# Performance work log

Measured on AMD Instinct MI355X. Metric: run time of the kernel, lower is better.

The kernel has to match this reference:

```python
import jax, jax.numpy as jnp
import numpy as np


def _gcn_conv(x, W, b, src, dst, norm, n_nodes):
    # PyG GCNConv: h = x @ W, then symmetric-normalized aggregation, then + b
    h = x @ W                                   # [N, F_out]
    msg = h[src] * norm[:, None]                # gather + scale, [E', F_out]
    agg = jax.ops.segment_sum(msg, dst, num_segments=n_nodes)
    return agg + b


def _norm_and_loops(edge_index, n_nodes):
    # add self-loops, compute D^{-1/2} (A+I) D^{-1/2} edge weights
    loop = jnp.arange(n_nodes, dtype=edge_index.dtype)
    src = jnp.concatenate([edge_index[0], loop])
    dst = jnp.concatenate([edge_index[1], loop])
    deg = jax.ops.segment_sum(jnp.ones_like(dst, dtype=jnp.float32), dst,
                              num_segments=n_nodes)
    dinv = jnp.where(deg > 0, jax.lax.rsqrt(deg), 0.0)
    norm = dinv[src] * dinv[dst]
    return src, dst, norm


def setup_inputs() -> dict:
    key = jax.random.key(0)
    ks = jax.random.split(key, 4)
    N, E, n_latent, n_dim = 50000, 800000, 128, 128
    hidden = 2 * n_latent
    x = jax.random.normal(ks[0], (N, n_latent), dtype=jnp.float32)
    edge_index = jax.random.randint(ks[1], (2, E), 0, N, dtype=jnp.int64)
    W1 = jax.random.normal(ks[2], (n_latent, hidden), dtype=jnp.float32) / np.sqrt(n_latent)
    b1 = jnp.zeros((hidden,), dtype=jnp.float32)
    W2 = jax.random.normal(ks[3], (hidden, n_dim), dtype=jnp.float32) / np.sqrt(hidden)
    b2 = jnp.zeros((n_dim,), dtype=jnp.float32)
    return {"x": x, "edge_index": edge_index, "W1": W1, "b1": b1,
            "W2": W2, "b2": b2}


def reference(x, edge_index, W1, b1, W2, b2):
    n_nodes = x.shape[0]
    src, dst, norm = _norm_and_loops(edge_index, n_nodes)
    z1 = jax.nn.relu(_gcn_conv(x, W1, b1, src, dst, norm, n_nodes))
    z2 = _gcn_conv(z1, W2, b2, src, dst, norm, n_nodes)
    return z2
```

## Files before the change

kernel.cpp:

```cpp
#include <hip/hip_runtime.h>


constexpr int F = 128;
constexpr int HID = 256;
constexpr int ECHUNK = 8192;

typedef __attribute__((ext_vector_type(8))) _Float16 f16x8;
typedef __attribute__((ext_vector_type(4))) _Float16 f16x4;
typedef __attribute__((ext_vector_type(2))) _Float16 f16x2;
typedef __attribute__((ext_vector_type(4))) float f32x4;

__global__ __launch_bounds__(256) void k_bzero(unsigned* bcnt) {
  bcnt[threadIdx.x] = 0u;
}

__global__ __launch_bounds__(256) void k_binc(const int* __restrict__ dst,
                                              unsigned* __restrict__ bcnt,
                                              unsigned* __restrict__ bhist, int E) {
  __shared__ unsigned hist[256];
  int tid = threadIdx.x;
  hist[tid] = 0u;
  __syncthreads();
  int i0 = blockIdx.x * ECHUNK;
  int i1 = min(i0 + ECHUNK, E);
  for (int i = i0 + tid; i < i1; i += 256)
    atomicAdd(&hist[((unsigned)dst[i]) >> 8], 1u);
  __syncthreads();
  unsigned c = hist[tid];
  bhist[blockIdx.x * 256 + tid] = c;
  if (c) atomicAdd(&bcnt[tid], c);
}

__global__ __launch_bounds__(256) void k_bscan(const unsigned* __restrict__ bcnt,
                                               unsigned* __restrict__ bbase,
                                               unsigned* __restrict__ bcur,
                                               int* __restrict__ rowptr,
                                               int P, int N, int E) {
  __shared__ unsigned wsum[4];
  int tid = threadIdx.x;
  unsigned v = (tid < P) ? bcnt[tid] : 0u;
  unsigned sv = v;
#pragma unroll
  for (int off = 1; off < 64; off <<= 1) {
    unsigned t = __shfl_up(sv, off);
    if ((tid & 63) >= off) sv += t;
  }
  int w = tid >> 6;
  if ((tid & 63) == 63) wsum[w] = sv;
  __syncthreads();
  unsigned wpre = 0;
  for (int k = 0; k < w; ++k) wpre += wsum[k];
  unsigned excl = wpre + sv - v;
  if (tid < P) {
    bbase[tid] = excl;
    bcur[tid] = excl;
  }
  if (tid == P - 1) bbase[P] = excl + v;
  if (tid == 0) rowptr[N] = E;
}

__global__ __launch_bounds__(256) void k_binscat(const int* __restrict__ src,
                                                 const int* __restrict__ dst,
                                                 const unsigned* __restrict__ bhist,
                                                 unsigned* __restrict__ bcur,
                                                 unsigned* __restrict__ packed, int E) {
  __shared__ unsigned hist[256];
  __shared__ unsigned basel[256];
  int tid = threadIdx.x;
  unsigned c = bhist[blockIdx.x * 256 + tid];
  if (c) basel[tid] = atomicAdd(&bcur[tid], c);
  hist[tid] = 0u;
  __syncthreads();
  int i0 = blockIdx.x * ECHUNK;
  int i1 = min(i0 + ECHUNK, E);
  for (int i = i0 + tid; i < i1; i += 256) {
    unsigned d = (unsigned)dst[i];
    unsigned b = d >> 8;
    unsigned pos = basel[b] + atomicAdd(&hist[b], 1u);
    packed[pos] = ((unsigned)src[i]) | ((d & 255u) << 16);
  }
}

__global__ __launch_bounds__(256) void k_bcsr(const unsigned* __restrict__ packed,
                                              const unsigned* __restrict__ bbase,
                                              float* __restrict__ dinv,
                                              int* __restrict__ rowptr,
                                              int* __restrict__ esrc, int N) {
  __shared__ unsigned hist[256];
  __shared__ unsigned rowloc[256];
  __shared__ unsigned cur[256];
  __shared__ unsigned wsum[4];
  int tid = threadIdx.x, b = blockIdx.x;
  int e0 = (int)bbase[b], e1 = (int)bbase[b + 1];
  hist[tid] = 0u;
  __syncthreads();
  for (int i = e0 + tid; i < e1; i += 256)
    atomicAdd(&hist[packed[i] >> 16], 1u);
  __syncthreads();
  unsigned v = hist[tid];
  unsigned sv = v;
#pragma unroll
  for (int off = 1; off < 64; off <<= 1) {
    unsigned t = __shfl_up(sv, off);
    if ((tid & 63) >= off) sv += t;
  }
  int w = tid >> 6;
  if ((tid & 63) == 63) wsum[w] = sv;
  __syncthreads();
  unsigned wpre = 0;
  for (int k = 0; k < w; ++k) wpre += wsum[k];
  unsigned excl = wpre + sv - v;
  int node = b * 256 + tid;
  if (node < N) {
    dinv[node] = rsqrtf((float)v + 1.0f);
    rowptr[node] = e0 + (int)excl;
  }
  rowloc[tid] = (unsigned)e0 + excl;
  cur[tid] = 0u;
  __syncthreads();
  for (int i = e0 + tid; i < e1; i += 256) {
    unsigned pk = packed[i];
    unsigned dl = pk >> 16;
    unsigned pos = rowloc[dl] + atomicAdd(&cur[dl], 1u);
    esrc[pos] = (int)(pk & 0xffffu);
  }
}

__global__ __launch_bounds__(256) void k_toh(const float* __restrict__ in,
                                             _Float16* __restrict__ outp, int n4) {
  int i = blockIdx.x * 256 + threadIdx.x;
  if (i >= n4) return;
  float4 v = ((const float4*)in)[i];
  f16x4 o;
  o.x = (_Float16)v.x; o.y = (_Float16)v.y;
  o.z = (_Float16)v.z; o.w = (_Float16)v.w;
  ((f16x4*)outp)[i] = o;
}

__global__ __launch_bounds__(256) void k_wcvt(const float* __restrict__ W,
                                              _Float16* __restrict__ Wt,
                                              int K, int Nn) {
  int idx = blockIdx.x * 256 + threadIdx.x;
  if (idx >= K * Nn) return;
  int k = idx / Nn, n = idx - k * Nn;
  Wt[n * K + k] = (_Float16)W[idx];
}

__global__ __launch_bounds__(256) void k_agg1(const int* __restrict__ rowptr,
                                              const int* __restrict__ esrc,
                                              const float* __restrict__ dinv,
                                              const float* __restrict__ xf,
                                              const _Float16* __restrict__ xh,
                                              _Float16* __restrict__ outp, int N) {
  int node = blockIdx.x * 4 + (threadIdx.x >> 6);
  int lane = threadIdx.x & 63;
  if (node >= N) return;
  float di = dinv[node];
  float w0 = di * di;
  float2 acc = ((const float2*)(xf + (size_t)node * F))[lane];
  acc.x *= w0; acc.y *= w0;
  int beg = rowptr[node], end = rowptr[node + 1];
  for (int b = beg; b < end; b += 64) {
    int n = min(64, end - b);
    int s = 0;
    float w = 0.f;
    if (lane < n) {
      s = esrc[b + lane];
      w = dinv[s] * di;
    }
    int t = 0;
    for (; t + 7 < n; t += 8) {
      int ss[8];
      float wz[8];
#pragma unroll
      for (int j = 0; j < 8; ++j) {
        ss[j] = __shfl(s, t + j);
        wz[j] = __shfl(w, t + j);
      }
      f16x2 vv[8];
#pragma unroll
      for (int j = 0; j < 8; ++j)
        vv[j] = ((const f16x2*)(xh + (size_t)ss[j] * F))[lane];
#pragma unroll
      for (int j = 0; j < 8; ++j) {
        acc.x += (float)vv[j].x * wz[j];
        acc.y += (float)vv[j].y * wz[j];
      }
    }
    for (; t < n; ++t) {
      int s0 = __shfl(s, t);
      float wa = __shfl(w, t);
      f16x2 v0 = ((const f16x2*)(xh + (size_t)s0 * F))[lane];
      acc.x += (float)v0.x * wa;
      acc.y += (float)v0.y * wa;
    }
  }
  f16x2 ov;
  ov.x = (_Float16)acc.x;
  ov.y = (_Float16)acc.y;
  ((f16x2*)(outp + (size_t)node * F))[lane] = ov;
}

__global__ __launch_bounds__(256) void k_agg_out(const int* __restrict__ rowptr,
                                                 const int* __restrict__ esrc,
                                                 const float* __restrict__ dinv,
                                                 const _Float16* __restrict__ hb,
                                                 const float* __restrict__ bias,
                                                 float* __restrict__ outp, int N) {
  int node = blockIdx.x * 4 + (threadIdx.x >> 6);
  int lane = threadIdx.x & 63;
  if (node >= N) return;
  float di = dinv[node];
  float w0 = di * di;
  f16x2 sv2 = ((const f16x2*)(hb + (size_t)node * F))[lane];
  float2 bb = ((const float2*)bias)[lane];
  float2 acc;
  acc.x = (float)sv2.x * w0 + bb.x;
  acc.y = (float)sv2.y * w0 + bb.y;
  int beg = rowptr[node], end = rowptr[node + 1];
  for (int b = beg; b < end; b += 64) {
    int n = min(64, end - b);
    int s = 0;
    float w = 0.f;
    if (lane < n) {
      s = esrc[b + lane];
      w = dinv[s] * di;
    }
    int t = 0;
    for (; t + 7 < n; t += 8) {
      int ss[8];
      float wz[8];
#pragma unroll
      for (int j = 0; j < 8; ++j) {
        ss[j] = __shfl(s, t + j);
        wz[j] = __shfl(w, t + j);
      }
      f16x2 vv[8];
#pragma unroll
      for (int j = 0; j < 8; ++j)
        vv[j] = ((const f16x2*)(hb + (size_t)ss[j] * F))[lane];
#pragma unroll
      for (int j = 0; j < 8; ++j) {
        acc.x += (float)vv[j].x * wz[j];
        acc.y += (float)vv[j].y * wz[j];
      }
    }
    for (; t < n; ++t) {
      int s0 = __shfl(s, t);
      float wa = __shfl(w, t);
      f16x2 v0 = ((const f16x2*)(hb + (size_t)s0 * F))[lane];
      acc.x += (float)v0.x * wa;
      acc.y += (float)v0.y * wa;
    }
  }
  ((float2*)(outp + (size_t)node * F))[lane] = acc;
}

__global__ __launch_bounds__(256) void k_gemm1(const _Float16* __restrict__ A,
                                               const _Float16* __restrict__ Bt,
                                               const float* __restrict__ bias,
                                               _Float16* __restrict__ C, int M) {
  __shared__ _Float16 AL[64 * 128];
  int tid = threadIdx.x;
  int lane = tid & 63, wid = tid >> 6;
  int row0 = blockIdx.x * 64;

#pragma unroll
  for (int i = 0; i < 4; ++i) {
    int g = i * 256 + tid;
    int r = g >> 4, gi = g & 15;
    int o = r * 128 + ((gi ^ (r & 7)) * 8);
    size_t go = (size_t)(row0 + r) * 128 + gi * 8;
    *(f16x8*)&AL[o] = *(const f16x8*)&A[go];
  }
  __syncthreads();

  f32x4 acc[4][4] = {};
#pragma unroll
  for (int ks = 0; ks < 4; ++ks) {
    f16x8 ah[4], bh[4];
#pragma unroll
    for (int mf = 0; mf < 4; ++mf) {
      int r = mf * 16 + (lane & 15);
      int g = ks * 4 + (lane >> 4);
      int o = r * 128 + ((g ^ (r & 7)) * 8);
      ah[mf] = *(const f16x8*)&AL[o];
    }
#pragma unroll
    for (int nf = 0; nf < 4; ++nf) {
      int c = wid * 64 + nf * 16 + (lane & 15);
      size_t o = (size_t)c * 128 + ks * 32 + (lane >> 4) * 8;
      bh[nf] = *(const f16x8*)&Bt[o];
    }
#pragma unroll
    for (int mf = 0; mf < 4; ++mf)
#pragma unroll
      for (int nf = 0; nf < 4; ++nf)
        acc[mf][nf] = __builtin_amdgcn_mfma_f32_16x16x32_f16(
            ah[mf], bh[nf], acc[mf][nf], 0, 0, 0);
  }

#pragma unroll
  for (int mf = 0; mf < 4; ++mf) {
    int r0 = row0 + mf * 16 + (lane >> 4) * 4;
#pragma unroll
    for (int nf = 0; nf < 4; ++nf) {
      int c = wid * 64 + nf * 16 + (lane & 15);
      float bv = bias[c];
#pragma unroll
      for (int r = 0; r < 4; ++r) {
        if (r0 + r < M) {
          float v = fmaxf(acc[mf][nf][r] + bv, 0.f);
          C[(size_t)(r0 + r) * HID + c] = (_Float16)v;
        }
      }
    }
  }
}

__global__ __launch_bounds__(256) void k_gemm2(const _Float16* __restrict__ Z,
                                               const _Float16* __restrict__ Bt,
                                               _Float16* __restrict__ C, int M) {
  __shared__ _Float16 ZL[64 * 256];
  int tid = threadIdx.x;
  int lane = tid & 63, wid = tid >> 6;
  int row0 = blockIdx.x * 64;

#pragma unroll
  for (int i = 0; i < 8; ++i) {
    int g = i * 256 + tid;
    int r = g >> 5, gi = g & 31;
    int o = r * 256 + ((gi ^ (r & 7)) * 8);
    size_t go = (size_t)(row0 + r) * 256 + gi * 8;
    *(f16x8*)&ZL[o] = *(const f16x8*)&Z[go];
  }
  __syncthreads();

  f32x4 acc[4][2] = {};
#pragma unroll
  for (int ks = 0; ks < 8; ++ks) {
    f16x8 ah[4], bh[2];
#pragma unroll
    for (int mf = 0; mf < 4; ++mf) {
      int r = mf * 16 + (lane & 15);
      int g = ks * 4 + (lane >> 4);
      int o = r * 256 + ((g ^ (r & 7)) * 8);
      ah[mf] = *(const f16x8*)&ZL[o];
    }
#pragma unroll
    for (int nf = 0; nf < 2; ++nf) {
      int c = wid * 32 + nf * 16 + (lane & 15);
      size_t o = (size_t)c * 256 + ks * 32 + (lane >> 4) * 8;
      bh[nf] = *(const f16x8*)&Bt[o];
    }
#pragma unroll
    for (int mf = 0; mf < 4; ++mf)
#pragma unroll
      for (int nf = 0; nf < 2; ++nf)
        acc[mf][nf] = __builtin_amdgcn_mfma_f32_16x16x32_f16(
            ah[mf], bh[nf], acc[mf][nf], 0, 0, 0);
  }

#pragma unroll
  for (int mf = 0; mf < 4; ++mf) {
    int r0 = row0 + mf * 16 + (lane >> 4) * 4;
#pragma unroll
    for (int nf = 0; nf < 2; ++nf) {
      int c = wid * 32 + nf * 16 + (lane & 15);
#pragma unroll
      for (int r = 0; r < 4; ++r)
        if (r0 + r < M) C[(size_t)(r0 + r) * F + c] = (_Float16)acc[mf][nf][r];
    }
  }
}

extern "C" void kernel_launch(void* const* d_in, const int* in_sizes, int n_in,
                              void* d_out, int out_size, void* d_ws, size_t ws_size,
                              hipStream_t stream) {
  const float* x = (const float*)d_in[0];
  const int* ei = (const int*)d_in[1];
  const float* W1 = (const float*)d_in[2];
  const float* b1 = (const float*)d_in[3];
  const float* W2 = (const float*)d_in[4];
  const float* b2 = (const float*)d_in[5];
  float* out = (float*)d_out;

  int N = in_sizes[0] / F;
  int E = in_sizes[1] / 2;
  const int* src = ei;
  const int* dst = ei + E;
  int P = (N + 255) / 256;
  int nbC = (E + ECHUNK - 1) / ECHUNK;

  char* ws = (char*)d_ws;
  size_t off = 0;
  auto allocB = [&](size_t bytes) {
    void* p = ws + off;
    off += ((bytes + 255) & ~(size_t)255);
    return p;
  };
  float* dinv = (float*)allocB((size_t)N * 4);
  int* rowptr = (int*)allocB(((size_t)N + 1) * 4);
  unsigned* bcnt = (unsigned*)allocB(256 * 4);
  unsigned* bbase = (unsigned*)allocB(257 * 4);
  unsigned* bcur = (unsigned*)allocB(256 * 4);
  unsigned* bhist = (unsigned*)allocB((size_t)nbC * 256 * 4);
  unsigned* packed = (unsigned*)allocB((size_t)E * 4);
  int* esrc = (int*)allocB((size_t)E * 4);
  _Float16* xh = (_Float16*)allocB((size_t)N * F * 2);
  _Float16* agg = (_Float16*)allocB((size_t)(N + 64) * F * 2);
  _Float16* z1 = (_Float16*)allocB((size_t)(N + 64) * HID * 2);
  _Float16* w1t = (_Float16*)allocB((size_t)F * HID * 2);
  _Float16* w2t = (_Float16*)allocB((size_t)HID * F * 2);
  _Float16* h2 = agg;

  int nbW = (F * HID + 255) / 256;
  int nbX = (N * F / 4 + 255) / 256;

  k_wcvt<<<nbW, 256, 0, stream>>>(W1, w1t, F, HID);
  k_wcvt<<<nbW, 256, 0, stream>>>(W2, w2t, HID, F);
  k_toh<<<nbX, 256, 0, stream>>>(x, xh, N * F / 4);

  k_bzero<<<1, 256, 0, stream>>>(bcnt);
  k_binc<<<nbC, 256, 0, stream>>>(dst, bcnt, bhist, E);
  k_bscan<<<1, 256, 0, stream>>>(bcnt, bbase, bcur, rowptr, P, N, E);
  k_binscat<<<nbC, 256, 0, stream>>>(src, dst, bhist, bcur, packed, E);
  k_bcsr<<<P, 256, 0, stream>>>(packed, bbase, dinv, rowptr, esrc, N);

  int nbAgg = (N + 3) / 4;
  int mb = (N + 63) / 64;

  k_agg1<<<nbAgg, 256, 0, stream>>>(rowptr, esrc, dinv, x, xh, agg, N);
  k_gemm1<<<mb, 256, 0, stream>>>(agg, w1t, b1, z1, N);

  k_gemm2<<<mb, 256, 0, stream>>>(z1, w2t, h2, N);
  k_agg_out<<<nbAgg, 256, 0, stream>>>(rowptr, esrc, dinv, h2, b2, out, N);
}
```

Before: 170.4 us.

## Split wavefront into two edge halves with 8-byte gathers and merge prep kernels

Both aggregation kernels now have each half-wavefront (32 lanes) process alternate edges with f16x4 loads covering the full 128-feature row. Partial sums are combined through a cross-half shuffle before the write, so each load instruction moves twice the bytes and two edges are fetched concurrently. The three conversion kernels are fused into one prep launch, and the zeroing kernel is replaced by hipMemsetAsync to cut launches. The self-loop term now reads from the fp16 copy instead of fp32 x, which slightly lowers precision. The cost is an extra reduction shuffle and half the lanes sitting idle at the store.

Measured after the change: 168.4 us. About the same (-1.2%).

```diff
diff --git a/kernel.cpp b/kernel.cpp
--- a/kernel.cpp
+++ b/kernel.cpp
@@ -7,12 +7,7 @@
 
 typedef __attribute__((ext_vector_type(8))) _Float16 f16x8;
 typedef __attribute__((ext_vector_type(4))) _Float16 f16x4;
-typedef __attribute__((ext_vector_type(2))) _Float16 f16x2;
 typedef __attribute__((ext_vector_type(4))) float f32x4;
-
-__global__ __launch_bounds__(256) void k_bzero(unsigned* bcnt) {
-  bcnt[threadIdx.x] = 0u;
-}
 
 __global__ __launch_bounds__(256) void k_binc(const int* __restrict__ dst,
                                               unsigned* __restrict__ bcnt,
@@ -126,39 +121,46 @@
   }
 }
 
-__global__ __launch_bounds__(256) void k_toh(const float* __restrict__ in,
-                                             _Float16* __restrict__ outp, int n4) {
-  int i = blockIdx.x * 256 + threadIdx.x;
-  if (i >= n4) return;
-  float4 v = ((const float4*)in)[i];
-  f16x4 o;
-  o.x = (_Float16)v.x; o.y = (_Float16)v.y;
-  o.z = (_Float16)v.z; o.w = (_Float16)v.w;
-  ((f16x4*)outp)[i] = o;
-}
-
-__global__ __launch_bounds__(256) void k_wcvt(const float* __restrict__ W,
-                                              _Float16* __restrict__ Wt,
-                                              int K, int Nn) {
-  int idx = blockIdx.x * 256 + threadIdx.x;
-  if (idx >= K * Nn) return;
-  int k = idx / Nn, n = idx - k * Nn;
-  Wt[n * K + k] = (_Float16)W[idx];
+__global__ __launch_bounds__(256) void k_prep(const float* __restrict__ W1,
+                                              const float* __restrict__ W2,
+                                              const float* __restrict__ x,
+                                              _Float16* __restrict__ w1t,
+                                              _Float16* __restrict__ w2t,
+                                              _Float16* __restrict__ xh, int n4) {
+  int b = blockIdx.x;
+  if (b < 128) {
+    int idx = b * 256 + threadIdx.x;
+    int k = idx / HID, n = idx - k * HID;
+    w1t[n * F + k] = (_Float16)W1[idx];
+  } else if (b < 256) {
+    int idx = (b - 128) * 256 + threadIdx.x;
+    int k = idx / F, n = idx - k * F;
+    w2t[n * HID + k] = (_Float16)W2[idx];
+  } else {
+    int i = (b - 256) * 256 + threadIdx.x;
+    if (i < n4) {
+      float4 v = ((const float4*)x)[i];
+      f16x4 o;
+      o.x = (_Float16)v.x; o.y = (_Float16)v.y;
+      o.z = (_Float16)v.z; o.w = (_Float16)v.w;
+      ((f16x4*)xh)[i] = o;
+    }
+  }
 }
 
 __global__ __launch_bounds__(256) void k_agg1(const int* __restrict__ rowptr,
                                               const int* __restrict__ esrc,
                                               const float* __restrict__ dinv,
-                                              const float* __restrict__ xf,
                                               const _Float16* __restrict__ xh,
                                               _Float16* __restrict__ outp, int N) {
   int node = blockIdx.x * 4 + (threadIdx.x >> 6);
   int lane = threadIdx.x & 63;
+  int li = lane & 31, hi = lane >> 5;
   if (node >= N) return;
   float di = dinv[node];
   float w0 = di * di;
-  float2 acc = ((const float2*)(xf + (size_t)node * F))[lane];
-  acc.x *= w0; acc.y *= w0;
+  f16x4 sv = ((const f16x4*)(xh + (size_t)node * F))[li];
+  float4 acc = make_float4(0.f, 0.f, 0.f, 0.f);
   int beg = rowptr[node], end = rowptr[node + 1];
   for (int b = beg; b < end; b += 64) {
     int n = min(64, end - b);
@@ -169,36 +171,50 @@
       w = dinv[s] * di;
     }
     int t = 0;
-    for (; t + 7 < n; t += 8) {
+    for (; t + 15 < n; t += 16) {
       int ss[8];
       float wz[8];
 #pragma unroll
       for (int j = 0; j < 8; ++j) {
-        ss[j] = __shfl(s, t + j);
-        wz[j] = __shfl(w, t + j);
+        int idx = t + 2 * j + hi;
+        ss[j] = __shfl(s, idx);
+        wz[j] = __shfl(w, idx);
       }
-      f16x2 vv[8];
+      f16x4 vv[8];
 #pragma unroll
       for (int j = 0; j < 8; ++j)
-        vv[j] = ((const f16x2*)(xh + (size_t)ss[j] * F))[lane];
+        vv[j] = ((const f16x4*)(xh + (size_t)ss[j] * F))[li];
 #pragma unroll
       for (int j = 0; j < 8; ++j) {
         acc.x += (float)vv[j].x * wz[j];
         acc.y += (float)vv[j].y * wz[j];
+        acc.z += (float)vv[j].z * wz[j];
+        acc.w += (float)vv[j].w * wz[j];
       }
     }
-    for (; t < n; ++t) {
-      int s0 = __shfl(s, t);
-      float wa = __shfl(w, t);
-      f16x2 v0 = ((const f16x2*)(xh + (size_t)s0 * F))[lane];
+    for (; t < n; t += 2) {
+      int idx = t + hi;
+      int s0 = __shfl(s, idx);
+      float wa = __shfl(w, idx);
+      f16x4 v0 = ((const f16x4*)(xh + (size_t)s0 * F))[li];
       acc.x += (float)v0.x * wa;
       acc.y += (float)v0.y * wa;
-    }
-  }
-  f16x2 ov;
-  ov.x = (_Float16)acc.x;
-  ov.y = (_Float16)acc.y;
-  ((f16x2*)(outp + (size_t)node * F))[lane] = ov;
+      acc.z += (float)v0.z * wa;
+      acc.w += (float)v0.w * wa;
+    }
+  }
+  acc.x += __shfl_xor(acc.x, 32);
+  acc.y += __shfl_xor(acc.y, 32);
+  acc.z += __shfl_xor(acc.z, 32);
+  acc.w += __shfl_xor(acc.w, 32);
+  if (hi == 0) {
+    f16x4 ov;
+    ov.x = (_Float16)(acc.x + (float)sv.x * w0);
+    ov.y = (_Float16)(acc.y + (float)sv.y * w0);
+    ov.z = (_Float16)(acc.z + (float)sv.z * w0);
+    ov.w = (_Float16)(acc.w + (float)sv.w * w0);
+    ((f16x4*)(outp + (size_t)node * F))[li] = ov;
+  }
 }
 
 __global__ __launch_bounds__(256) void k_agg_out(const int* __restrict__ rowptr,
@@ -209,14 +225,12 @@
                                                  float* __restrict__ outp, int N) {
   int node = blockIdx.x * 4 + (threadIdx.x >> 6);
   int lane = threadIdx.x & 63;
+  int li = lane & 31, hi = lane >> 5;
   if (node >= N) return;
   float di = dinv[node];
   float w0 = di * di;
-  f16x2 sv2 = ((const f16x2*)(hb + (size_t)node * F))[lane];
-  float2 bb = ((const float2*)bias)[lane];
-  float2 acc;
-  acc.x = (float)sv2.x * w0 + bb.x;
-  acc.y = (float)sv2.y * w0 + bb.y;
+  f16x4 sv = ((const f16x4*)(hb + (size_t)node * F))[li];
+  float4 acc = make_float4(0.f, 0.f, 0.f, 0.f);
   int beg = rowptr[node], end = rowptr[node + 1];
   for (int b = beg; b < end; b += 64) {
     int n = min(64, end - b);
@@ -227,33 +241,51 @@
       w = dinv[s] * di;
     }
     int t = 0;
-    for (; t + 7 < n; t += 8) {
+    for (; t + 15 < n; t += 16) {
       int ss[8];
       float wz[8];
 #pragma unroll
       for (int j = 0; j < 8; ++j) {
-        ss[j] = __shfl(s, t + j);
-        wz[j] = __shfl(w, t + j);
+        int idx = t + 2 * j + hi;
+        ss[j] = __shfl(s, idx);
+        wz[j] = __shfl(w, idx);
       }
-      f16x2 vv[8];
+      f16x4 vv[8];
 #pragma unroll
       for (int j = 0; j < 8; ++j)
-        vv[j] = ((const f16x2*)(hb + (size_t)ss[j] * F))[lane];
+        vv[j] = ((const f16x4*)(hb + (size_t)ss[j] * F))[li];
 #pragma unroll
       for (int j = 0; j < 8; ++j) {
         acc.x += (float)vv[j].x * wz[j];
         acc.y += (float)vv[j].y * wz[j];
+        acc.z += (float)vv[j].z * wz[j];
+        acc.w += (float)vv[j].w * wz[j];
       }
     }
-    for (; t < n; ++t) {
-      int s0 = __shfl(s, t);
-      float wa = __shfl(w, t);
-      f16x2 v0 = ((const f16x2*)(hb + (size_t)s0 * F))[lane];
+    for (; t < n; t += 2) {
+      int idx = t + hi;
+      int s0 = __shfl(s, idx);
+      float wa = __shfl(w, idx);
+      f16x4 v0 = ((const f16x4*)(hb + (size_t)s0 * F))[li];
       acc.x += (float)v0.x * wa;
       acc.y += (float)v0.y * wa;
-    }
-  }
-  ((float2*)(outp + (size_t)node * F))[lane] = acc;
+      acc.z += (float)v0.z * wa;
+      acc.w += (float)v0.w * wa;
+    }
+  }
+  acc.x += __shfl_xor(acc.x, 32);
+  acc.y += __shfl_xor(acc.y, 32);
+  acc.z += __shfl_xor(acc.z, 32);
+  acc.w += __shfl_xor(acc.w, 32);
+  if (hi == 0) {
+    float4 bb = ((const float4*)bias)[li];
+    float4 ov;
+    ov.x = acc.x + (float)sv.x * w0 + bb.x;
+    ov.y = acc.y + (float)sv.y * w0 + bb.y;
+    ov.z = acc.z + (float)sv.z * w0 + bb.z;
+    ov.w = acc.w + (float)sv.w * w0 + bb.w;
+    ((float4*)(outp + (size_t)node * F))[li] = ov;
+  }
 }
 
 __global__ __launch_bounds__(256) void k_gemm1(const _Float16* __restrict__ A,
@@ -414,14 +446,12 @@
   _Float16* w2t = (_Float16*)allocB((size_t)HID * F * 2);
   _Float16* h2 = agg;
 
-  int nbW = (F * HID + 255) / 256;
-  int nbX = (N * F / 4 + 255) / 256;
-
-  k_wcvt<<<nbW, 256, 0, stream>>>(W1, w1t, F, HID);
-  k_wcvt<<<nbW, 256, 0, stream>>>(W2, w2t, HID, F);
-  k_toh<<<nbX, 256, 0, stream>>>(x, xh, N * F / 4);
-
-  k_bzero<<<1, 256, 0, stream>>>(bcnt);
+  int n4 = N * F / 4;
+  int nbPrep = 256 + (n4 + 255) / 256;
+
+  k_prep<<<nbPrep, 256, 0, stream>>>(W1, W2, x, w1t, w2t, xh, n4);
+
+  hipMemsetAsync(bcnt, 0, 256 * 4, stream);
   k_binc<<<nbC, 256, 0, stream>>>(dst, bcnt, bhist, E);
   k_bscan<<<1, 256, 0, stream>>>(bcnt, bbase, bcur, rowptr, P, N, E);
   k_binscat<<<nbC, 256, 0, stream>>>(src, dst, bhist, bcur, packed, E);
@@ -430,7 +460,7 @@
   int nbAgg = (N + 3) / 4;
   int mb = (N + 63) / 64;
 
-  k_agg1<<<nbAgg, 256, 0, stream>>>(rowptr, esrc, dinv, x, xh, agg, N);
+  k_agg1<<<nbAgg, 256, 0, stream>>>(rowptr, esrc, dinv, xh, agg, N);
   k_gemm1<<<mb, 256, 0, stream>>>(agg, w1t, b1, z1, N);
 
   k_gemm2<<<mb, 256, 0, stream>>>(z1, w2t, h2, N);
```

## Aggregate with 16 lanes per node using 16-byte loads; fuse prep kernels

Applied to the files above, without the earlier changes.

Both aggregation kernels now give each node 16 lanes that load 8 halves per gather, where before a full 64-lane wave per node loaded 2 halves. This puts 16 nodes in a block, raises bytes per load and memory-level parallelism, and adds a 4-wide tail loop. The weight and feature fp16 conversions and the bucket histogram are merged into one launch, and a memset replaces the zeroing kernel, to cut launch overhead. The first layer's self term now reads the fp16 copy of x instead of fp32, which slightly lowers precision.

Measured after the change: 168.8 us. About the same (-1.0%).

```diff
diff --git a/kernel.cpp b/kernel.cpp
--- a/kernel.cpp
+++ b/kernel.cpp
@@ -7,28 +7,50 @@
 
 typedef __attribute__((ext_vector_type(8))) _Float16 f16x8;
 typedef __attribute__((ext_vector_type(4))) _Float16 f16x4;
-typedef __attribute__((ext_vector_type(2))) _Float16 f16x2;
 typedef __attribute__((ext_vector_type(4))) float f32x4;
 
-__global__ __launch_bounds__(256) void k_bzero(unsigned* bcnt) {
-  bcnt[threadIdx.x] = 0u;
-}
-
-__global__ __launch_bounds__(256) void k_binc(const int* __restrict__ dst,
+__global__ __launch_bounds__(256) void k_prep(const int* __restrict__ dst,
                                               unsigned* __restrict__ bcnt,
-                                              unsigned* __restrict__ bhist, int E) {
+                                              unsigned* __restrict__ bhist,
+                                              const float* __restrict__ W1,
+                                              const float* __restrict__ W2,
+                                              const float* __restrict__ x,
+                                              _Float16* __restrict__ w1t,
+                                              _Float16* __restrict__ w2t,
+                                              _Float16* __restrict__ xh,
+                                              int E, int nbC, int n4) {
   __shared__ unsigned hist[256];
+  int b = blockIdx.x;
   int tid = threadIdx.x;
-  hist[tid] = 0u;
-  __syncthreads();
-  int i0 = blockIdx.x * ECHUNK;
-  int i1 = min(i0 + ECHUNK, E);
-  for (int i = i0 + tid; i < i1; i += 256)
-    atomicAdd(&hist[((unsigned)dst[i]) >> 8], 1u);
-  __syncthreads();
-  unsigned c = hist[tid];
-  bhist[blockIdx.x * 256 + tid] = c;
-  if (c) atomicAdd(&bcnt[tid], c);
+  if (b < nbC) {
+    hist[tid] = 0u;
+    __syncthreads();
+    int i0 = b * ECHUNK;
+    int i1 = min(i0 + ECHUNK, E);
+    for (int i = i0 + tid; i < i1; i += 256)
+      atomicAdd(&hist[((unsigned)dst[i]) >> 8], 1u);
+    __syncthreads();
+    unsigned c = hist[tid];
+    bhist[b * 256 + tid] = c;
+    if (c) atomicAdd(&bcnt[tid], c);
+  } else if (b < nbC + 128) {
+    int idx = (b - nbC) * 256 + tid;
+    int k = idx / HID, n = idx - k * HID;
+    w1t[n * F + k] = (_Float16)W1[idx];
+  } else if (b < nbC + 256) {
+    int idx = (b - nbC - 128) * 256 + tid;
+    int k = idx / F, n = idx - k * F;
+    w2t[n * HID + k] = (_Float16)W2[idx];
+  } else {
+    int i = (b - nbC - 256) * 256 + tid;
+    if (i < n4) {
+      float4 v = ((const float4*)x)[i];
+      f16x4 o;
+      o.x = (_Float16)v.x; o.y = (_Float16)v.y;
+      o.z = (_Float16)v.z; o.w = (_Float16)v.w;
+      ((f16x4*)xh)[i] = o;
+    }
+  }
 }
 
 __global__ __launch_bounds__(256) void k_bscan(const unsigned* __restrict__ bcnt,
@@ -126,46 +148,26 @@
   }
 }
 
-__global__ __launch_bounds__(256) void k_toh(const float* __restrict__ in,
-                                             _Float16* __restrict__ outp, int n4) {
-  int i = blockIdx.x * 256 + threadIdx.x;
-  if (i >= n4) return;
-  float4 v = ((const float4*)in)[i];
-  f16x4 o;
-  o.x = (_Float16)v.x; o.y = (_Float16)v.y;
-  o.z = (_Float16)v.z; o.w = (_Float16)v.w;
-  ((f16x4*)outp)[i] = o;
-}
-
-__global__ __launch_bounds__(256) void k_wcvt(const float* __restrict__ W,
-                                              _Float16* __restrict__ Wt,
-                                              int K, int Nn) {
-  int idx = blockIdx.x * 256 + threadIdx.x;
-  if (idx >= K * Nn) return;
-  int k = idx / Nn, n = idx - k * Nn;
-  Wt[n * K + k] = (_Float16)W[idx];
-}
-
 __global__ __launch_bounds__(256) void k_agg1(const int* __restrict__ rowptr,
                                               const int* __restrict__ esrc,
                                               const float* __restrict__ dinv,
-                                              const float* __restrict__ xf,
                                               const _Float16* __restrict__ xh,
                                               _Float16* __restrict__ outp, int N) {
-  int node = blockIdx.x * 4 + (threadIdx.x >> 6);
-  int lane = threadIdx.x & 63;
+  int node = blockIdx.x * 16 + (threadIdx.x >> 4);
+  int li = threadIdx.x & 15;
+  int lanebase = (threadIdx.x & 63) & 48;
   if (node >= N) return;
   float di = dinv[node];
   float w0 = di * di;
-  float2 acc = ((const float2*)(xf + (size_t)node * F))[lane];
-  acc.x *= w0; acc.y *= w0;
+  f16x8 svv = ((const f16x8*)(xh + (size_t)node * F))[li];
+  float acc[8] = {};
   int beg = rowptr[node], end = rowptr[node + 1];
-  for (int b = beg; b < end; b += 64) {
-    int n = min(64, end - b);
+  for (int b = beg; b < end; b += 16) {
+    int n = min(16, end - b);
     int s = 0;
     float w = 0.f;
-    if (lane < n) {
-      s = esrc[b + lane];
+    if (li < n) {
+      s = esrc[b + li];
       w = dinv[s] * di;
     }
     int t = 0;
@@ -174,31 +176,49 @@
       float wz[8];
 #pragma unroll
       for (int j = 0; j < 8; ++j) {
-        ss[j] = __shfl(s, t + j);
-        wz[j] = __shfl(w, t + j);
+        ss[j] = __shfl(s, lanebase + t + j);
+        wz[j] = __shfl(w, lanebase + t + j);
       }
-      f16x2 vv[8];
+      f16x8 vv[8];
 #pragma unroll
       for (int j = 0; j < 8; ++j)
-        vv[j] = ((const f16x2*)(xh + (size_t)ss[j] * F))[lane];
-#pragma unroll
-      for (int j = 0; j < 8; ++j) {
-        acc.x += (float)vv[j].x * wz[j];
-        acc.y += (float)vv[j].y * wz[j];
+        vv[j] = ((const f16x8*)(xh + (size_t)ss[j] * F))[li];
+#pragma unroll
+      for (int j = 0; j < 8; ++j)
+#pragma unroll
+        for (int k = 0; k < 8; ++k)
+          acc[k] += (float)vv[j][k] * wz[j];
+    }
+    for (; t + 3 < n; t += 4) {
+      int ss[4];
+      float wz[4];
+#pragma unroll
+      for (int j = 0; j < 4; ++j) {
+        ss[j] = __shfl(s, lanebase + t + j);
+        wz[j] = __shfl(w, lanebase + t + j);
       }
+      f16x8 vv[4];
+#pragma unroll
+      for (int j = 0; j < 4; ++j)
+        vv[j] = ((const f16x8*)(xh + (size_t)ss[j] * F))[li];
+#pragma unroll
+      for (int j = 0; j < 4; ++j)
+#pragma unroll
+        for (int k = 0; k < 8; ++k)
+          acc[k] += (float)vv[j][k] * wz[j];
     }
     for (; t < n; ++t) {
-      int s0 = __shfl(s, t);
-      float wa = __shfl(w, t);
-      f16x2 v0 = ((const f16x2*)(xh + (size_t)s0 * F))[lane];
-      acc.x += (float)v0.x * wa;
-      acc.y += (float)v0.y * wa;
-    }
-  }
-  f16x2 ov;
-  ov.x = (_Float16)acc.x;
-  ov.y = (_Float16)acc.y;
-  ((f16x2*)(outp + (size_t)node * F))[lane] = ov;
+      int s0 = __shfl(s, lanebase + t);
+      float wa = __shfl(w, lanebase + t);
+      f16x8 v0 = ((const f16x8*)(xh + (size_t)s0 * F))[li];
+#pragma unroll
+      for (int k = 0; k < 8; ++k) acc[k] += (float)v0[k] * wa;
+    }
+  }
+  f16x8 ov;
+#pragma unroll
+  for (int k = 0; k < 8; ++k) ov[k] = (_Float16)(acc[k] + (float)svv[k] * w0);
+  ((f16x8*)(outp + (size_t)node * F))[li] = ov;
 }
 
 __global__ __launch_bounds__(256) void k_agg_out(const int* __restrict__ rowptr,
@@ -207,23 +227,21 @@
                                                  const _Float16* __restrict__ hb,
                                                  const float* __restrict__ bias,
                                                  float* __restrict__ outp, int N) {
-  int node = blockIdx.x * 4 + (threadIdx.x >> 6);
-  int lane = threadIdx.x & 63;
+  int node = blockIdx.x * 16 + (threadIdx.x >> 4);
+  int li = threadIdx.x & 15;
+  int lanebase = (threadIdx.x & 63) & 48;
   if (node >= N) return;
   float di = dinv[node];
   float w0 = di * di;
-  f16x2 sv2 = ((const f16x2*)(hb + (size_t)node * F))[lane];
-  float2 bb = ((const float2*)bias)[lane];
-  float2 acc;
-  acc.x = (float)sv2.x * w0 + bb.x;
-  acc.y = (float)sv2.y * w0 + bb.y;
+  f16x8 svv = ((const f16x8*)(hb + (size_t)node * F))[li];
+  float acc[8] = {};
   int beg = rowptr[node], end = rowptr[node + 1];
-  for (int b = beg; b < end; b += 64) {
-    int n = min(64, end - b);
+  for (int b = beg; b < end; b += 16) {
+    int n = min(16, end - b);
     int s = 0;
     float w = 0.f;
-    if (lane < n) {
-      s = esrc[b + lane];
+    if (li < n) {
+      s = esrc[b + li];
       w = dinv[s] * di;
     }
     int t = 0;
@@ -232,28 +250,59 @@
       float wz[8];
 #pragma unroll
       for (int j = 0; j < 8; ++j) {
-        ss[j] = __shfl(s, t + j);
-        wz[j] = __shfl(w, t + j);
+        ss[j] = __shfl(s, lanebase + t + j);
+        wz[j] = __shfl(w, lanebase + t + j);
       }
-      f16x2 vv[8];
+      f16x8 vv[8];
 #pragma unroll
       for (int j = 0; j < 8; ++j)
-        vv[j] = ((const f16x2*)(hb + (size_t)ss[j] * F))[lane];
-#pragma unroll
-      for (int j = 0; j < 8; ++j) {
-        acc.x += (float)vv[j].x * wz[j];
-        acc.y += (float)vv[j].y * wz[j];
+        vv[j] = ((const f16x8*)(hb + (size_t)ss[j] * F))[li];
+#pragma unroll
+      for (int j = 0; j < 8; ++j)
+#pragma unroll
+        for (int k = 0; k < 8; ++k)
+          acc[k] += (float)vv[j][k] * wz[j];
+    }
+    for (; t + 3 < n; t += 4) {
+      int ss[4];
+      float wz[4];
+#pragma unroll
+      for (int j = 0; j < 4; ++j) {
+        ss[j] = __shfl(s, lanebase + t + j);
+        wz[j] = __shfl(w, lanebase + t + j);
       }
+      f16x8 vv[4];
+#pragma unroll
+      for (int j = 0; j < 4; ++j)
+        vv[j] = ((const f16x8*)(hb + (size_t)ss[j] * F))[li];
+#pragma unroll
+      for (int j = 0; j < 4; ++j)
+#pragma unroll
+        for (int k = 0; k < 8; ++k)
+          acc[k] += (float)vv[j][k] * wz[j];
     }
     for (; t < n; ++t) {
-      int s0 = __shfl(s, t);
-      float wa = __shfl(w, t);
-      f16x2 v0 = ((const f16x2*)(hb + (size_t)s0 * F))[lane];
-      acc.x += (float)v0.x * wa;
-      acc.y += (float)v0.y * wa;
-    }
-  }
-  ((float2*)(outp + (size_t)node * F))[lane] = acc;
+      int s0 = __shfl(s, lanebase + t);
+      float wa = __shfl(w, lanebase + t);
+      f16x8 v0 = ((const f16x8*)(hb + (size_t)s0 * F))[li];
+#pragma unroll
+      for (int k = 0; k < 8; ++k) acc[k] += (float)v0[k] * wa;
+    }
+  }
+  float4 bb0 = ((const float4*)bias)[li * 2];
+  float4 bb1 = ((const float4*)bias)[li * 2 + 1];
+  float4 o0, o1;
+  o0.x = acc[0] + (float)svv[0] * w0 + bb0.x;
+  o0.y = acc[1] + (float)svv[1] * w0 + bb0.y;
+  o0.z = acc[2] + (float)svv[2] * w0 + bb0.z;
+  o0.w = acc[3] + (float)svv[3] * w0 + bb0.w;
+  o1.x = acc[4] + (float)svv[4] * w0 + bb1.x;
+  o1.y = acc[5] + (float)svv[5] * w0 + bb1.y;
+  o1.z = acc[6] + (float)svv[6] * w0 + bb1.z;
+  o1.w = acc[7] + (float)svv[7] * w0 + bb1.w;
+  float* orow = outp + (size_t)node * F + li * 8;
+  *(float4*)orow = o0;
+  *(float4*)(orow + 4) = o1;
 }
 
 __global__ __launch_bounds__(256) void k_gemm1(const _Float16* __restrict__ A,
@@ -414,23 +463,20 @@
   _Float16* w2t = (_Float16*)allocB((size_t)HID * F * 2);
   _Float16* h2 = agg;
 
-  int nbW = (F * HID + 255) / 256;
-  int nbX = (N * F / 4 + 255) / 256;
-
-  k_wcvt<<<nbW, 256, 0, stream>>>(W1, w1t, F, HID);
-  k_wcvt<<<nbW, 256, 0, stream>>>(W2, w2t, HID, F);
-  k_toh<<<nbX, 256, 0, stream>>>(x, xh, N * F / 4);
-
-  k_bzero<<<1, 256, 0, stream>>>(bcnt);
-  k_binc<<<nbC, 256, 0, stream>>>(dst, bcnt, bhist, E);
+  int n4 = N * F / 4;
+  int nbPrep = nbC + 256 + (n4 + 255) / 256;
+
+  hipMemsetAsync(bcnt, 0, 256 * 4, stream);
+  k_prep<<<nbPrep, 256, 0, stream>>>(dst, bcnt, bhist, W1, W2, x, w1t, w2t, xh,
+                                     E, nbC, n4);
   k_bscan<<<1, 256, 0, stream>>>(bcnt, bbase, bcur, rowptr, P, N, E);
   k_binscat<<<nbC, 256, 0, stream>>>(src, dst, bhist, bcur, packed, E);
   k_bcsr<<<P, 256, 0, stream>>>(packed, bbase, dinv, rowptr, esrc, N);
 
-  int nbAgg = (N + 3) / 4;
+  int nbAgg = (N + 15) / 16;
   int mb = (N + 63) / 64;
 
-  k_agg1<<<nbAgg, 256, 0, stream>>>(rowptr, esrc, dinv, x, xh, agg, N);
+  k_agg1<<<nbAgg, 256, 0, stream>>>(rowptr, esrc, dinv, xh, agg, N);
   k_gemm1<<<mb, 256, 0, stream>>>(agg, w1t, b1, z1, N);
 
   k_gemm2<<<mb, 256, 0, stream>>>(z1, w2t, h2, N);
```
